# Kernel tuning notes

Measured on AMD Instinct MI355X. Metric: run time of the kernel, lower is better.

The kernel has to match this reference:

```python
import math
import jax, jax.numpy as jnp
import numpy as np

EMBED = 1024
INTERNAL = 1024  # EMBED // downsample_rate(=1)
HEADS = 16


def setup_inputs() -> dict:
    key = jax.random.key(0)
    ks = jax.random.split(key, 11)
    b, n, m = 2, 2048, 2048
    s = 1.0 / math.sqrt(EMBED)
    inp = {
        "q": jax.random.normal(ks[0], (b, n, EMBED), jnp.float32),
        "k": jax.random.normal(ks[1], (b, m, EMBED), jnp.float32),
        "v": jax.random.normal(ks[2], (b, m, EMBED), jnp.float32),
        # Linear params (torch Linear: y = x @ W.T + b); store as [in, out].
        "Wq": jax.random.normal(ks[3], (EMBED, INTERNAL), jnp.float32) * s,
        "bq": jax.random.normal(ks[4], (INTERNAL,), jnp.float32) * s,
        "Wk": jax.random.normal(ks[5], (EMBED, INTERNAL), jnp.float32) * s,
        "bk": jax.random.normal(ks[6], (INTERNAL,), jnp.float32) * s,
        "Wv": jax.random.normal(ks[7], (EMBED, INTERNAL), jnp.float32) * s,
        "bv": jax.random.normal(ks[8], (INTERNAL,), jnp.float32) * s,
        "Wo": jax.random.normal(ks[9], (INTERNAL, EMBED), jnp.float32) * s,
        "bo": jax.random.normal(ks[10], (EMBED,), jnp.float32) * s,
    }
    return inp


def _split_heads(x):  # [b, n, c] -> [b, h, n, c/h]
    b, n, c = x.shape
    return x.reshape(b, n, HEADS, c // HEADS).transpose(0, 2, 1, 3)


def reference(q, k, v, Wq, bq, Wk, bk, Wv, bv, Wo, bo):
    qh = _split_heads(q @ Wq + bq)
    kh = _split_heads(k @ Wk + bk)
    vh = _split_heads(v @ Wv + bv)
    c_per_head = kh.shape[-1]
    attn = jnp.einsum("bhnc,bhmc->bhnm", qh, kh) / math.sqrt(c_per_head)
    attn = jax.nn.softmax(attn, axis=-1)
    out = jnp.einsum("bhnm,bhmc->bhnc", attn, vh)
    b, h, n, ch = out.shape
    out = out.transpose(0, 2, 1, 3).reshape(b, n, h * ch)
    return out @ Wo + bo
```

## Files before the change

kernel.cpp:

```cpp
#include <hip/hip_runtime.h>

#define EMBED 1024
#define HEADS 16
#define DHEAD 64
#define BATCH 2
#define SEQ 2048
#define ROWS (BATCH*SEQ)
#define SZA (ROWS*EMBED)
#define SW (EMBED*EMBED)

typedef _Float16 f16;
typedef __attribute__((ext_vector_type(2))) __fp16 h16x2;
typedef __attribute__((ext_vector_type(4))) _Float16 f16x4;
typedef __attribute__((ext_vector_type(8))) _Float16 f16x8;
typedef __attribute__((ext_vector_type(4))) float f32x4;

__device__ __forceinline__ void gld16(const f16* g, f16* lds) {
  __builtin_amdgcn_global_load_lds(
      (const __attribute__((address_space(1))) void*)g,
      (__attribute__((address_space(3))) void*)lds, 16, 0, 0);
}

__global__ __launch_bounds__(256) void pre_kernel(
    const float* __restrict__ q, const float* __restrict__ k,
    const float* __restrict__ v, f16* __restrict__ qc,
    f16* __restrict__ kc, f16* __restrict__ vc,
    const float* __restrict__ w0, const float* __restrict__ w1,
    const float* __restrict__ w2, const float* __restrict__ w3,
    f16* __restrict__ o0, f16* __restrict__ o1,
    f16* __restrict__ o2, f16* __restrict__ o3) {
  __shared__ float tile[32][33];
  const int y = blockIdx.y;
  if (y < 3) {
    const float* in = y == 0 ? q : y == 1 ? k : v;
    f16* out       = y == 0 ? qc : y == 1 ? kc : vc;
    int i = blockIdx.x * 256 + threadIdx.x;
    float4 f = ((const float4* __restrict__)in)[i];
    union { f16 h[4]; short4 s4; } u;
    u.h[0] = (f16)f.x; u.h[1] = (f16)f.y; u.h[2] = (f16)f.z; u.h[3] = (f16)f.w;
    ((short4* __restrict__)out)[i] = u.s4;
    return;
  }
  const int x = blockIdx.x;
  const int z = x >> 10, by = (x >> 5) & 31, bx = x & 31;
  const float* in = z == 0 ? w0 : z == 1 ? w1 : z == 2 ? w2 : w3;
  f16* out       = z == 0 ? o0 : z == 1 ? o1 : z == 2 ? o2 : o3;
  int tx = threadIdx.x & 31, ty = threadIdx.x >> 5;
  #pragma unroll
  for (int i = 0; i < 32; i += 8)
    tile[ty + i][tx] = in[(by*32 + ty + i)*EMBED + bx*32 + tx];
  __syncthreads();
  #pragma unroll
  for (int i = 0; i < 32; i += 8)
    out[(bx*32 + ty + i)*EMBED + by*32 + tx] = (f16)tile[tx][ty + i];
}

__global__ __launch_bounds__(256) void gemm3_kernel(
    const f16* __restrict__ qc, const f16* __restrict__ kc, const f16* __restrict__ vc,
    const f16* __restrict__ Wqt, const f16* __restrict__ Wkt, const f16* __restrict__ Wvt,
    const float* __restrict__ bq, const float* __restrict__ bk, const float* __restrict__ bv,
    f16* __restrict__ Qp, f16* __restrict__ Kp, f16* __restrict__ Vtg) {
  __shared__ __align__(16) f16 As[128*32];
  __shared__ __align__(16) f16 Bs[128*32];
  const int z = blockIdx.y;
  const f16 *A, *Bt; const float* bias; f16* C;
  int mbase, nbase, N, biasrow;
  if (z == 0)      { A=qc;  Bt=Wqt; bias=bq; C=Qp;  mbase=(blockIdx.x&31)*128; nbase=(blockIdx.x>>5)*128; N=EMBED; biasrow=0; }
  else if (z == 1) { A=kc;  Bt=Wkt; bias=bk; C=Kp;  mbase=(blockIdx.x&31)*128; nbase=(blockIdx.x>>5)*128; N=EMBED; biasrow=0; }
  else             { A=Wvt; Bt=vc;  bias=bv; C=Vtg; mbase=(blockIdx.x&7)*128;  nbase=(blockIdx.x>>3)*128; N=ROWS;  biasrow=1; }
  const int K = EMBED;
  const int tid = threadIdx.x;
  const int wave = tid >> 6, lane = tid & 63;
  const int lg = lane >> 4, lr = lane & 15;
  const int wm = (wave >> 1) * 64, wn = (wave & 1) * 64;
  const int sr = lane >> 2;
  const int sc = ((lane & 3) ^ ((lane >> 3) & 3)) * 8;
  const f16* gA0 = A  + (size_t)(mbase + wave*16 + sr)*K + sc;
  const f16* gA1 = A  + (size_t)(mbase + 64 + wave*16 + sr)*K + sc;
  const f16* gB0 = Bt + (size_t)(nbase + wave*16 + sr)*K + sc;
  const f16* gB1 = Bt + (size_t)(nbase + 64 + wave*16 + sr)*K + sc;
  f16* lA0 = &As[(wave*16)*32];
  f16* lA1 = &As[(64 + wave*16)*32];
  f16* lB0 = &Bs[(wave*16)*32];
  f16* lB1 = &Bs[(64 + wave*16)*32];
  const int csw = (lg ^ ((lr >> 1) & 3)) * 8;
  f32x4 acc[4][4] = {};
  for (int k0 = 0; k0 < K; k0 += 32) {
    __syncthreads();
    gld16(gA0 + k0, lA0);
    gld16(gA1 + k0, lA1);
    gld16(gB0 + k0, lB0);
    gld16(gB1 + k0, lB1);
    __syncthreads();
    f16x8 af[4], bf[4];
    #pragma unroll
    for (int mt = 0; mt < 4; mt++)
      af[mt] = *(const f16x8*)&As[(wm + mt*16 + lr)*32 + csw];
    #pragma unroll
    for (int nt = 0; nt < 4; nt++)
      bf[nt] = *(const f16x8*)&Bs[(wn + nt*16 + lr)*32 + csw];
    #pragma unroll
    for (int mt = 0; mt < 4; mt++)
      #pragma unroll
      for (int nt = 0; nt < 4; nt++)
        acc[mt][nt] = __builtin_amdgcn_mfma_f32_16x16x32_f16(af[mt], bf[nt], acc[mt][nt], 0, 0, 0);
  }
  #pragma unroll
  for (int mt = 0; mt < 4; mt++)
    #pragma unroll
    for (int nt = 0; nt < 4; nt++)
      #pragma unroll
      for (int i = 0; i < 4; i++) {
        int row = mbase + wm + mt*16 + lg*4 + i;
        int col = nbase + wn + nt*16 + lr;
        float val = acc[mt][nt][i] + (biasrow ? bias[row] : bias[col]);
        if (z == 0) val *= 0.18033688011f;
        C[(size_t)row*N + col] = (f16)val;
      }
}

__global__ __launch_bounds__(256) void gemmo_kernel(
    const f16* __restrict__ A, const f16* __restrict__ Bt,
    const float* __restrict__ bias, float* __restrict__ Cf) {
  __shared__ __align__(16) f16 As[128*32];
  __shared__ __align__(16) f16 Bs[64*32];
  const int K = EMBED, N = EMBED;
  const int tid = threadIdx.x;
  const int wave = tid >> 6, lane = tid & 63;
  const int lg = lane >> 4, lr = lane & 15;
  const int mbase = blockIdx.x * 128, nbase = blockIdx.y * 64;
  const int wm = (wave >> 1) * 64, wn = (wave & 1) * 32;
  const int sr = wave*16 + (lane >> 2);
  const int sc = ((lane & 3) ^ ((lane >> 3) & 3)) * 8;
  const f16* gA0 = A  + (size_t)(mbase + sr)*K + sc;
  const f16* gA1 = A  + (size_t)(mbase + 64 + sr)*K + sc;
  const f16* gB  = Bt + (size_t)(nbase + sr)*K + sc;
  f16* lA0 = &As[(wave*16)*32];
  f16* lA1 = &As[(64 + wave*16)*32];
  f16* lB  = &Bs[(wave*16)*32];
  const int csw = (lg ^ ((lr >> 1) & 3)) * 8;
  f32x4 acc[4][2] = {};
  for (int k0 = 0; k0 < K; k0 += 32) {
    __syncthreads();
    gld16(gA0 + k0, lA0);
    gld16(gA1 + k0, lA1);
    gld16(gB  + k0, lB);
    __syncthreads();
    f16x8 af[4], bf[2];
    #pragma unroll
    for (int mt = 0; mt < 4; mt++)
      af[mt] = *(const f16x8*)&As[(wm + mt*16 + lr)*32 + csw];
    #pragma unroll
    for (int nt = 0; nt < 2; nt++)
      bf[nt] = *(const f16x8*)&Bs[(wn + nt*16 + lr)*32 + csw];
    #pragma unroll
    for (int mt = 0; mt < 4; mt++)
      #pragma unroll
      for (int nt = 0; nt < 2; nt++)
        acc[mt][nt] = __builtin_amdgcn_mfma_f32_16x16x32_f16(af[mt], bf[nt], acc[mt][nt], 0, 0, 0);
  }
  #pragma unroll
  for (int mt = 0; mt < 4; mt++)
    #pragma unroll
    for (int nt = 0; nt < 2; nt++)
      #pragma unroll
      for (int i = 0; i < 4; i++) {
        int row = mbase + wm + mt*16 + lg*4 + i;
        int col = nbase + wn + nt*16 + lr;
        Cf[(size_t)row*N + col] = acc[mt][nt][i] + bias[col];
      }
}

__global__ __launch_bounds__(256, 2) void attn_kernel(
    const f16* __restrict__ Qp, const f16* __restrict__ Kp,
    const f16* __restrict__ Vt, f16* __restrict__ Ob) {
  __shared__ __align__(16) f16 Ks[2*4096];
  __shared__ __align__(16) f16 Vs[2*4096];
  const int tid = threadIdx.x;
  const int wave = tid >> 6, lane = tid & 63;
  const int lg = lane >> 4, lr = lane & 15;
  const int gid = blockIdx.x;
  const int bh  = (gid & 7)*4 + ((gid >> 3) & 3);
  const int qblk = gid >> 5;
  const int h = bh & 15, b = bh >> 4;
  const int q0 = qblk*128 + wave*32;
  const f16* Qh = Qp + (size_t)b*SEQ*EMBED + h*DHEAD;
  const f16* Kh = Kp + (size_t)b*SEQ*EMBED + h*DHEAD;
  const f16* Vh = Vt + (size_t)h*DHEAD*ROWS + (size_t)b*SEQ;

  const f16* kst[2]; const f16* vst[2]; f16* kdst[2]; f16* vdst[2];
  #pragma unroll
  for (int m = 0; m < 2; m++) {
    int sgrp = m*4 + wave;
    int srow = sgrp*8 + (lane >> 3);
    int sch  = (lane & 7) ^ (srow & 7);
    int prow = ((srow>>5)&1)*32 + ((srow>>4)&1)*4 + ((srow>>2)&3)*8 + (srow&3);
    kst[m] = Kh + (size_t)prow*EMBED + sch*8;
    vst[m] = Vh + (size_t)srow*ROWS + sch*8;
    kdst[m] = &Ks[sgrp*512];
    vdst[m] = &Vs[sgrp*512];
  }

  f16x8 qf[2][2];
  #pragma unroll
  for (int qb = 0; qb < 2; qb++)
    #pragma unroll
    for (int ds = 0; ds < 2; ds++)
      qf[qb][ds] = *(const f16x8*)&Qh[(size_t)(q0 + qb*16 + lr)*EMBED + ds*32 + lg*8];

  const int c0 = ((lg)     ^ (lr & 7)) * 8;
  const int c1 = ((4 + lg) ^ (lr & 7)) * 8;

  f32x4 o[4][2] = {};
  f32x4 lacc[2] = {};
  f32x4 sa[2][4];
  f16x8 va[4][2];
  const f32x4 NEG8 = {-8.f, -8.f, -8.f, -8.f};
  f16x8 onesf;
  #pragma unroll
  for (int i = 0; i < 8; i++) onesf[i] = (f16)1.0f;

  auto STAGE = [&](int t, int po) {
    const size_t kt = (size_t)t * 64;
    gld16(kst[0] + kt*EMBED, kdst[0] + po);
    gld16(kst[1] + kt*EMBED, kdst[1] + po);
    gld16(vst[0] + kt, vdst[0] + po);
    gld16(vst[1] + kt, vdst[1] + po);
  };
  auto QK = [&](int bo, f32x4 (&s)[2][4]) {
    f16x8 ka[4][2];
    #pragma unroll
    for (int nb = 0; nb < 4; nb++) {
      ka[nb][0] = *(const f16x8*)&Ks[bo + (nb*16 + lr)*64 + c0];
      ka[nb][1] = *(const f16x8*)&Ks[bo + (nb*16 + lr)*64 + c1];
    }
    __builtin_amdgcn_s_setprio(1);
    #pragma unroll
    for (int nb = 0; nb < 4; nb++)
      #pragma unroll
      for (int qb = 0; qb < 2; qb++) {
        f32x4 z = __builtin_amdgcn_mfma_f32_16x16x32_f16(ka[nb][0], qf[qb][0], NEG8, 0, 0, 0);
        s[qb][nb] = __builtin_amdgcn_mfma_f32_16x16x32_f16(ka[nb][1], qf[qb][1], z, 0, 0, 0);
      }
    __builtin_amdgcn_s_setprio(0);
  };
  auto LDV = [&](int bo) {
    #pragma unroll
    for (int dm = 0; dm < 4; dm++) {
      va[dm][0] = *(const f16x8*)&Vs[bo + (dm*16 + lr)*64 + c0];
      va[dm][1] = *(const f16x8*)&Vs[bo + (dm*16 + lr)*64 + c1];
    }
  };
  auto SMPV = [&]() {
    f16x8 pf[2][2];
    #pragma unroll
    for (int qb = 0; qb < 2; qb++) {
      float p[4][4];
      #pragma unroll
      for (int nb = 0; nb < 4; nb++)
        #pragma unroll
        for (int i = 0; i < 4; i++)
          p[nb][i] = __builtin_amdgcn_exp2f(sa[qb][nb][i]);
      union { f16x8 v; h16x2 h2[4]; } u0, u1;
      u0.h2[0] = __builtin_amdgcn_cvt_pkrtz(p[0][0], p[0][1]);
      u0.h2[1] = __builtin_amdgcn_cvt_pkrtz(p[0][2], p[0][3]);
      u0.h2[2] = __builtin_amdgcn_cvt_pkrtz(p[1][0], p[1][1]);
      u0.h2[3] = __builtin_amdgcn_cvt_pkrtz(p[1][2], p[1][3]);
      u1.h2[0] = __builtin_amdgcn_cvt_pkrtz(p[2][0], p[2][1]);
      u1.h2[1] = __builtin_amdgcn_cvt_pkrtz(p[2][2], p[2][3]);
      u1.h2[2] = __builtin_amdgcn_cvt_pkrtz(p[3][0], p[3][1]);
      u1.h2[3] = __builtin_amdgcn_cvt_pkrtz(p[3][2], p[3][3]);
      pf[qb][0] = u0.v;
      pf[qb][1] = u1.v;
    }
    __builtin_amdgcn_s_setprio(1);
    #pragma unroll
    for (int ks = 0; ks < 2; ks++)
      #pragma unroll
      for (int qb = 0; qb < 2; qb++) {
        #pragma unroll
        for (int dm = 0; dm < 4; dm++)
          o[dm][qb] = __builtin_amdgcn_mfma_f32_16x16x32_f16(va[dm][ks], pf[qb][ks], o[dm][qb], 0, 0, 0);
        lacc[qb] = __builtin_amdgcn_mfma_f32_16x16x32_f16(onesf, pf[qb][ks], lacc[qb], 0, 0, 0);
      }
    __builtin_amdgcn_s_setprio(0);
  };

  STAGE(0, 0);
  __syncthreads();
  STAGE(1, 4096);
  QK(0, sa);
  LDV(0);
  __syncthreads();

  #pragma unroll 2
  for (int t = 1; t < 32; ++t) {
    const int bo = (t & 1) * 4096;
    if (t < 31) STAGE(t + 1, 4096 - bo);
    f32x4 sn[2][4];
    QK(bo, sn);
    SMPV();
    LDV(bo);
    #pragma unroll
    for (int qb = 0; qb < 2; qb++)
      #pragma unroll
      for (int nb = 0; nb < 4; nb++)
        sa[qb][nb] = sn[qb][nb];
    __syncthreads();
  }
  SMPV();

  const float inv[2] = { 1.f / lacc[0][0], 1.f / lacc[1][0] };

  #pragma unroll
  for (int qb = 0; qb < 2; qb++) {
    const size_t rowb = (size_t)(b*SEQ + q0 + qb*16 + lr)*EMBED + h*DHEAD;
    #pragma unroll
    for (int dm = 0; dm < 4; dm++) {
      f16x4 w;
      #pragma unroll
      for (int i = 0; i < 4; i++) w[i] = (f16)(o[dm][qb][i] * inv[qb]);
      *(f16x4*)&Ob[rowb + dm*16 + 4*lg] = w;
    }
  }
}

extern "C" void kernel_launch(void* const* d_in, const int* in_sizes, int n_in,
                              void* d_out, int out_size, void* d_ws, size_t ws_size,
                              hipStream_t stream) {
  (void)in_sizes; (void)n_in; (void)out_size; (void)ws_size;
  const float* q  = (const float*)d_in[0];
  const float* k  = (const float*)d_in[1];
  const float* v  = (const float*)d_in[2];
  const float* Wq = (const float*)d_in[3];
  const float* bq = (const float*)d_in[4];
  const float* Wk = (const float*)d_in[5];
  const float* bk = (const float*)d_in[6];
  const float* Wv = (const float*)d_in[7];
  const float* bv = (const float*)d_in[8];
  const float* Wo = (const float*)d_in[9];
  const float* bo = (const float*)d_in[10];
  float* out = (float*)d_out;

  f16* w   = (f16*)d_ws;
  f16* qc  = w;
  f16* kc  = qc + SZA;
  f16* vc  = kc + SZA;
  f16* Qp  = vc + SZA;
  f16* Kp  = Qp + SZA;
  f16* Vtg = Kp + SZA;
  f16* Ob  = Vtg + SZA;
  f16* Wqt = Ob + SZA;
  f16* Wkt = Wqt + SW;
  f16* Wvt = Wkt + SW;
  f16* Wot = Wvt + SW;

  dim3 pg(4096, 4);
  pre_kernel<<<pg, 256, 0, stream>>>(q, k, v, qc, kc, vc,
                                     Wq, Wk, Wv, Wo, Wqt, Wkt, Wvt, Wot);
  dim3 g3(256, 3);
  gemm3_kernel<<<g3, 256, 0, stream>>>(qc, kc, vc, Wqt, Wkt, Wvt, bq, bk, bv, Qp, Kp, Vtg);
  attn_kernel<<<512, 256, 0, stream>>>(Qp, Kp, Vtg, Ob);
  dim3 go(ROWS/128, EMBED/64);
  gemmo_kernel<<<go, 256, 0, stream>>>(Ob, Wot, bo, out);
}
```

Baseline: 211.2 us.

## Load K and V tiles directly from global memory into registers, dropping LDS staging

Removes the shared-memory double buffer and async global-to-LDS copies in the attention kernel, so each wave loads its K and V fragments straight from global memory into registers. This also removes the per-iteration block barriers. The loop is reordered so the next K load is issued before softmax/PV and the next V load before QK, hiding latency behind MFMA work. In exchange, each of the four waves now fetches the same K/V tile independently, which quadruples global/L2 traffic and uses uncoalesced 16-byte strided loads.

```diff
diff --git a/kernel.cpp b/kernel.cpp
--- a/kernel.cpp
+++ b/kernel.cpp
@@ -174,8 +174,6 @@
 __global__ __launch_bounds__(256, 2) void attn_kernel(
     const f16* __restrict__ Qp, const f16* __restrict__ Kp,
     const f16* __restrict__ Vt, f16* __restrict__ Ob) {
-  __shared__ __align__(16) f16 Ks[2*4096];
-  __shared__ __align__(16) f16 Vs[2*4096];
   const int tid = threadIdx.x;
   const int wave = tid >> 6, lane = tid & 63;
   const int lg = lane >> 4, lr = lane & 15;
@@ -188,18 +186,16 @@
   const f16* Kh = Kp + (size_t)b*SEQ*EMBED + h*DHEAD;
   const f16* Vh = Vt + (size_t)h*DHEAD*ROWS + (size_t)b*SEQ;
 
-  const f16* kst[2]; const f16* vst[2]; f16* kdst[2]; f16* vdst[2];
-  #pragma unroll
-  for (int m = 0; m < 2; m++) {
-    int sgrp = m*4 + wave;
-    int srow = sgrp*8 + (lane >> 3);
-    int sch  = (lane & 7) ^ (srow & 7);
-    int prow = ((srow>>5)&1)*32 + ((srow>>4)&1)*4 + ((srow>>2)&3)*8 + (srow&3);
-    kst[m] = Kh + (size_t)prow*EMBED + sch*8;
-    vst[m] = Vh + (size_t)srow*ROWS + sch*8;
-    kdst[m] = &Ks[sgrp*512];
-    vdst[m] = &Vs[sgrp*512];
-  }
+  const f16* kp[4]; const f16* vp[4];
+  #pragma unroll
+  for (int nb = 0; nb < 4; nb++) {
+    int r = nb*16 + lr;
+    int prow = ((r>>5)&1)*32 + ((r>>4)&1)*4 + ((r>>2)&3)*8 + (r&3);
+    kp[nb] = Kh + (size_t)prow*EMBED + lg*8;
+  }
+  #pragma unroll
+  for (int dm = 0; dm < 4; dm++)
+    vp[dm] = Vh + (size_t)(dm*16 + lr)*ROWS + lg*8;
 
   f16x8 qf[2][2];
   #pragma unroll
@@ -207,33 +203,34 @@
     #pragma unroll
     for (int ds = 0; ds < 2; ds++)
       qf[qb][ds] = *(const f16x8*)&Qh[(size_t)(q0 + qb*16 + lr)*EMBED + ds*32 + lg*8];
-
-  const int c0 = ((lg)     ^ (lr & 7)) * 8;
-  const int c1 = ((4 + lg) ^ (lr & 7)) * 8;
 
   f32x4 o[4][2] = {};
   f32x4 lacc[2] = {};
   f32x4 sa[2][4];
+  f16x8 ka[4][2];
   f16x8 va[4][2];
   const f32x4 NEG8 = {-8.f, -8.f, -8.f, -8.f};
   f16x8 onesf;
   #pragma unroll
   for (int i = 0; i < 8; i++) onesf[i] = (f16)1.0f;
 
-  auto STAGE = [&](int t, int po) {
-    const size_t kt = (size_t)t * 64;
-    gld16(kst[0] + kt*EMBED, kdst[0] + po);
-    gld16(kst[1] + kt*EMBED, kdst[1] + po);
-    gld16(vst[0] + kt, vdst[0] + po);
-    gld16(vst[1] + kt, vdst[1] + po);
+  auto LDK = [&](int t) {
+    const size_t off = (size_t)t * 64 * EMBED;
+    #pragma unroll
+    for (int nb = 0; nb < 4; nb++) {
+      ka[nb][0] = *(const f16x8*)(kp[nb] + off);
+      ka[nb][1] = *(const f16x8*)(kp[nb] + off + 32);
+    }
   };
-  auto QK = [&](int bo, f32x4 (&s)[2][4]) {
-    f16x8 ka[4][2];
-    #pragma unroll
-    for (int nb = 0; nb < 4; nb++) {
-      ka[nb][0] = *(const f16x8*)&Ks[bo + (nb*16 + lr)*64 + c0];
-      ka[nb][1] = *(const f16x8*)&Ks[bo + (nb*16 + lr)*64 + c1];
+  auto LDV = [&](int t) {
+    const size_t off = (size_t)t * 64;
+    #pragma unroll
+    for (int dm = 0; dm < 4; dm++) {
+      va[dm][0] = *(const f16x8*)(vp[dm] + off);
+      va[dm][1] = *(const f16x8*)(vp[dm] + off + 32);
     }
+  };
+  auto QK = [&](f32x4 (&s)[2][4]) {
     __builtin_amdgcn_s_setprio(1);
     #pragma unroll
     for (int nb = 0; nb < 4; nb++)
@@ -243,13 +240,6 @@
         s[qb][nb] = __builtin_amdgcn_mfma_f32_16x16x32_f16(ka[nb][1], qf[qb][1], z, 0, 0, 0);
       }
     __builtin_amdgcn_s_setprio(0);
-  };
-  auto LDV = [&](int bo) {
-    #pragma unroll
-    for (int dm = 0; dm < 4; dm++) {
-      va[dm][0] = *(const f16x8*)&Vs[bo + (dm*16 + lr)*64 + c0];
-      va[dm][1] = *(const f16x8*)&Vs[bo + (dm*16 + lr)*64 + c1];
-    }
   };
   auto SMPV = [&]() {
     f16x8 pf[2][2];
@@ -286,27 +276,22 @@
     __builtin_amdgcn_s_setprio(0);
   };
 
-  STAGE(0, 0);
-  __syncthreads();
-  STAGE(1, 4096);
-  QK(0, sa);
+  LDK(0);
   LDV(0);
-  __syncthreads();
+  QK(sa);
 
   #pragma unroll 2
   for (int t = 1; t < 32; ++t) {
-    const int bo = (t & 1) * 4096;
-    if (t < 31) STAGE(t + 1, 4096 - bo);
+    LDK(t);
+    SMPV();
+    LDV(t);
     f32x4 sn[2][4];
-    QK(bo, sn);
-    SMPV();
-    LDV(bo);
+    QK(sn);
     #pragma unroll
     for (int qb = 0; qb < 2; qb++)
       #pragma unroll
       for (int nb = 0; nb < 4; nb++)
         sa[qb][nb] = sn[qb][nb];
-    __syncthreads();
   }
   SMPV();
 
```

Measured after the change: 286.6 us. +35.7%, slower.
